# Optimization experiments

Measured on AMD Instinct MI355X. Metric: run time of the kernel, lower is better.

## Reference

```python
import jax, jax.numpy as jnp
import numpy as np
import math

B, N, DIN, H, D, M, K, E = 1, 30000, 128, 4, 64, 64, 6, 480000
TAU = 0.25
EPS = 1e-6  # numerical_stabilizer in softmax_kernel_transformation


def _make_projection(m, d, seed=0):
    # FAVOR+ projection: stacked QR-orthogonalized blocks, rows rescaled by
    # norms of iid gaussian rows (scaling == 0 branch of create_projection_matrix).
    rng = np.random.default_rng(seed)
    blocks, rows = [], 0
    while rows < m:
        q, _ = np.linalg.qr(rng.standard_normal((d, d)))
        blocks.append(q.T[: min(d, m - rows)])
        rows += d
    mat = np.vstack(blocks)
    mult = np.linalg.norm(rng.standard_normal((m, d)), axis=1)
    return jnp.asarray(mult[:, None] * mat, dtype=jnp.float32)


def setup_inputs() -> dict:
    key = jax.random.key(0)
    ks = jax.random.split(key, 10)
    f32 = jnp.float32
    return {
        "z": jax.random.normal(ks[0], (B, N, DIN), dtype=f32),
        "Wq_w": jax.random.normal(ks[1], (DIN, H * D), dtype=f32) * DIN ** -0.5,
        "Wq_b": jnp.zeros((H * D,), f32),
        "Wk_w": jax.random.normal(ks[2], (DIN, H * D), dtype=f32) * DIN ** -0.5,
        "Wk_b": jnp.zeros((H * D,), f32),
        "Wv_w": jax.random.normal(ks[3], (DIN, H * D), dtype=f32) * DIN ** -0.5,
        "Wv_b": jnp.zeros((H * D,), f32),
        "Wo_w": jax.random.normal(ks[4], (H * D, D), dtype=f32) * (H * D) ** -0.5,
        "Wo_b": jnp.zeros((D,), f32),
        "proj": _make_projection(M, D),
        "gumbels": jax.random.gumbel(ks[5], (N, B, H, K), dtype=f32),
        "edge_index": jax.random.randint(ks[6], (2, E), 0, N),
    }


def _softmax_kernel(data, proj, is_query):
    # softmax_kernel_transformation: positive random features for exp kernel.
    dn = 1.0 / jnp.sqrt(jnp.sqrt(jnp.asarray(data.shape[-1], data.dtype)))
    data = data * dn  # [B,N,H,D]
    ratio = 1.0 / jnp.sqrt(jnp.asarray(proj.shape[0], data.dtype))
    dd = jnp.einsum("bnhd,md->bnhm", data, proj)
    diag = jnp.sum(data * data, axis=-1, keepdims=True) * 0.5
    if is_query:
        mx = jnp.max(dd, axis=-1, keepdims=True)            # per-row max
    else:
        mx = jnp.max(dd, axis=(1, 3), keepdims=True)        # max over n and m
    return ratio * (jnp.exp(dd - diag - mx) + EPS)


def reference(z, Wq_w, Wq_b, Wk_w, Wk_b, Wv_w, Wv_b, Wo_w, Wo_b, proj, gumbels, edge_index):
    inv_sqrt_tau = 1.0 / math.sqrt(TAU)
    q = (z @ Wq_w + Wq_b).reshape(B, N, H, D) * inv_sqrt_tau
    k = (z @ Wk_w + Wk_b).reshape(B, N, H, D) * inv_sqrt_tau
    v = (z @ Wv_w + Wv_b).reshape(B, N, H, D)

    qp = jnp.transpose(_softmax_kernel(q, proj, True), (1, 0, 2, 3))   # [N,B,H,M]
    kp = jnp.transpose(_softmax_kernel(k, proj, False), (1, 0, 2, 3))  # [N,B,H,M]
    v = jnp.transpose(v, (1, 0, 2, 3))                                  # [N,B,H,D]

    g = gumbels / TAU                                                   # [N,B,H,K]
    kt = kp[:, :, :, None, :] * jnp.exp(g)[..., None]                   # [N,B,H,K,M]

    kvs = jnp.einsum("nbhkm,nbhd->bhkmd", kt, v)
    z_num = jnp.einsum("nbhm,bhkmd->nbhkd", qp, kvs)                    # [N,B,H,K,D]
    ks_sum = jnp.sum(kt, axis=0)                                        # [B,H,K,M]
    z_den = jnp.einsum("nbhm,bhkm->nbhk", qp, ks_sum)                   # [N,B,H,K]
    z_out = jnp.mean(z_num / z_den[..., None], axis=3)                  # [N,B,H,D]
    z_out = jnp.transpose(z_out, (1, 0, 2, 3))                          # [B,N,H,D]

    # edge attention weights (for edge loss), non-gumbel normalizer
    start, end = edge_index[0], edge_index[1]
    edge_num = jnp.einsum("ebhm,ebhm->ebh", qp[end], kp[start])         # [E,B,H]
    norm = jnp.einsum("nbhm,bhm->nbh", qp, jnp.sum(kp, axis=0))         # [N,B,H]
    A_weight = jnp.transpose(edge_num / norm[end], (1, 0, 2))           # [B,E,H]

    z_next = z_out.reshape(B, N, H * D) @ Wo_w + Wo_b                   # [B,N,D]
    return z_next, A_weight
```

## Files before the change

### kernel.cpp

```cpp
#include <hip/hip_runtime.h>
#include <hip/hip_bf16.h>

#define NN   30000
#define DIN  128
#define NHD  256
#define HH   4
#define DD   64
#define MM   64
#define KK   6
#define EE   480000
#define ZOFF 1920000
#define NCS   125
#define CHUNK 240
#define PITCH  30208
#define PITCH4 3776

typedef __attribute__((ext_vector_type(8))) short bf16x8;
typedef __attribute__((ext_vector_type(4))) float f32x4;
typedef __attribute__((ext_vector_type(2))) float f32x2;

__device__ __forceinline__ unsigned f2key(float f) {
    unsigned u = __float_as_uint(f);
    return (u & 0x80000000u) ? ~u : (u | 0x80000000u);
}
__device__ __forceinline__ float key2f(unsigned k) {
    return __uint_as_float((k & 0x80000000u) ? (k ^ 0x80000000u) : ~k);
}
__device__ __forceinline__ unsigned short f2bf(float f) {
    unsigned u = __float_as_uint(f);
    unsigned r = ((u >> 16) & 1u) + 0x7fffu;
    return (unsigned short)((u + r) >> 16);
}
__device__ __forceinline__ float bf2f(unsigned short u) {
    return __uint_as_float((unsigned)u << 16);
}
__device__ __forceinline__ unsigned char ftofp8(float x) {
    unsigned u = __float_as_uint(x);
    int e32 = (int)(u >> 23) - 127;
    if (e32 <= -7) {
        int m = (int)rintf(x * 512.f);
        return (unsigned char)m;
    }
    unsigned r = ((u >> 20) & 1u) + 0x7FFFFu;
    u += r;
    e32 = (int)(u >> 23) - 127;
    if (e32 > 8) return 0x7E;
    int m = (u >> 20) & 7;
    return (unsigned char)(((e32 + 7) << 3) | m);
}
__device__ __forceinline__ float fp8tof(unsigned char u) {
    int e = (u >> 3) & 15, m = u & 7;
    if (e == 0) return (float)m * 0.001953125f;
    return __uint_as_float((unsigned)((e + 120) << 23) | ((unsigned)m << 20));
}
__device__ __forceinline__ void fp8x4tof(unsigned w, float* o) {
#if __has_builtin(__builtin_amdgcn_cvt_pk_f32_fp8)
    f32x2 lo = __builtin_amdgcn_cvt_pk_f32_fp8((int)w, false);
    f32x2 hi = __builtin_amdgcn_cvt_pk_f32_fp8((int)w, true);
    o[0] = lo[0]; o[1] = lo[1]; o[2] = hi[0]; o[3] = hi[1];
#else
    o[0] = fp8tof((unsigned char)(w & 255));
    o[1] = fp8tof((unsigned char)((w >> 8) & 255));
    o[2] = fp8tof((unsigned char)((w >> 16) & 255));
    o[3] = fp8tof((unsigned char)((w >> 24) & 255));
#endif
}

__global__ void init_kernel(unsigned* gmax) {
    if (threadIdx.x < HH) gmax[threadIdx.x] = 0u;
}

__global__ __launch_bounds__(256) void zcast_kernel(
    const float* __restrict__ z, unsigned short* __restrict__ zh) {
    int idx = blockIdx.x * 256 + threadIdx.x;
    float4 v = ((const float4*)z)[idx];
    ushort4 u;
    u.x = f2bf(v.x); u.y = f2bf(v.y); u.z = f2bf(v.z); u.w = f2bf(v.w);
    ((ushort4*)zh)[idx] = u;
}

__global__ __launch_bounds__(256) void wtransp_kernel(
    const float* __restrict__ Wq, const float* __restrict__ Wk,
    const float* __restrict__ Wv, unsigned short* __restrict__ WT) {
    __shared__ unsigned short tl[64][72];
    const int t = threadIdx.x;
    const int kt = blockIdx.x & 1, ct = blockIdx.x >> 1;
    const int wi = blockIdx.y;
    const float* W = (wi == 0) ? Wq : (wi == 1) ? Wk : Wv;
    const float4* W4 = (const float4*)W;
    #pragma unroll
    for (int it = 0; it < 4; ++it) {
        int idx = t + it * 256;
        int r = idx >> 4, c4 = idx & 15;
        float4 v = W4[(kt * 64 + r) * 64 + ct * 16 + c4];
        tl[c4 * 4 + 0][r] = f2bf(v.x);
        tl[c4 * 4 + 1][r] = f2bf(v.y);
        tl[c4 * 4 + 2][r] = f2bf(v.z);
        tl[c4 * 4 + 3][r] = f2bf(v.w);
    }
    __syncthreads();
    uint4* d4 = (uint4*)WT;
    #pragma unroll
    for (int it = 0; it < 2; ++it) {
        int idx = t + it * 256;
        int m = idx >> 3, g = idx & 7;
        d4[((size_t)wi * 256 + ct * 64 + m) * 16 + kt * 8 + g] = *(uint4*)&tl[m][g * 8];
    }
}

__global__ void projcast_kernel(const float* __restrict__ proj,
                                unsigned short* __restrict__ projh) {
    int i = blockIdx.x * 256 + threadIdx.x;
    projh[i] = f2bf(proj[i] * 0.35355339059327373f);
}

__global__ __launch_bounds__(256) void qkv_mfma_kernel(
    const unsigned short* __restrict__ zh, const unsigned short* __restrict__ WT,
    const float* __restrict__ bq, const float* __restrict__ bk, const float* __restrict__ bv,
    unsigned short* __restrict__ qh, unsigned short* __restrict__ kh,
    unsigned short* __restrict__ vh) {
    __shared__ __align__(16) unsigned short zt[128 * 128];
    __shared__ __align__(16) unsigned short wt[64 * 128];
    const int t = threadIdx.x;
    const int n0 = blockIdx.x * 128;
    const int wi = blockIdx.y;
    const float sc = (wi == 2) ? 1.0f : 2.0f;
    const float* bias = (wi == 0) ? bq : (wi == 1) ? bk : bv;
    unsigned short* outp = (wi == 0) ? qh : (wi == 1) ? kh : vh;
    const uint4* zg = (const uint4*)zh;
    #pragma unroll
    for (int it = 0; it < 8; ++it) {
        int idx = t + it * 256;
        int row = idx >> 4, g = idx & 15;
        int n = n0 + row;
        uint4 v = make_uint4(0u, 0u, 0u, 0u);
        if (n < NN) v = zg[(size_t)n * 16 + g];
        *(uint4*)&zt[row * 128 + ((g ^ (row & 7)) * 8)] = v;
    }
    const uint4* wg = (const uint4*)WT + (size_t)wi * 4096;
    const int w = t >> 6, lane = t & 63, lrow = lane & 15, lk = lane >> 4;
    for (int cc = 0; cc < 4; ++cc) {
        __syncthreads();
        #pragma unroll
        for (int it = 0; it < 4; ++it) {
            int idx = t + it * 256;
            int r = idx >> 4, g = idx & 15;
            *(uint4*)&wt[r * 128 + ((g ^ (r & 7)) * 8)] = wg[(cc * 64 + r) * 16 + g];
        }
        __syncthreads();
        f32x4 acc[4][2];
        #pragma unroll
        for (int mt = 0; mt < 4; ++mt) {
            acc[mt][0] = (f32x4){0.f, 0.f, 0.f, 0.f};
            acc[mt][1] = (f32x4){0.f, 0.f, 0.f, 0.f};
        }
        #pragma unroll
        for (int ks = 0; ks < 4; ++ks) {
            const int g0 = ks * 4 + lk;
            bf16x8 a[4], b[2];
            #pragma unroll
            for (int mt = 0; mt < 4; ++mt) {
                int r = mt * 16 + lrow;
                a[mt] = *(const bf16x8*)&wt[r * 128 + ((g0 ^ (r & 7)) * 8)];
            }
            #pragma unroll
            for (int nt = 0; nt < 2; ++nt) {
                int node = (w * 2 + nt) * 16 + lrow;
                b[nt] = *(const bf16x8*)&zt[node * 128 + ((g0 ^ (node & 7)) * 8)];
            }
            #pragma unroll
            for (int mt = 0; mt < 4; ++mt)
                #pragma unroll
                for (int nt = 0; nt < 2; ++nt)
                    acc[mt][nt] = __builtin_amdgcn_mfma_f32_16x16x32_bf16(
                        a[mt], b[nt], acc[mt][nt], 0, 0, 0);
        }
        #pragma unroll
        for (int mt = 0; mt < 4; ++mt) {
            int cbase = cc * 64 + mt * 16 + lk * 4;
            float4 bi = *(const float4*)&bias[cbase];
            #pragma unroll
            for (int nt = 0; nt < 2; ++nt) {
                int n = n0 + (w * 2 + nt) * 16 + lrow;
                if (n < NN) {
                    ushort4 u;
                    u.x = f2bf((acc[mt][nt][0] + bi.x) * sc);
                    u.y = f2bf((acc[mt][nt][1] + bi.y) * sc);
                    u.z = f2bf((acc[mt][nt][2] + bi.z) * sc);
                    u.w = f2bf((acc[mt][nt][3] + bi.w) * sc);
                    *(ushort4*)&outp[(size_t)n * NHD + cbase] = u;
                }
            }
        }
    }
}

__global__ __launch_bounds__(256) void feat_mfma_kernel(
    unsigned short* __restrict__ qbh, const unsigned short* __restrict__ kh,
    float* __restrict__ kb, const unsigned short* __restrict__ projh,
    unsigned* __restrict__ gmax) {
    __shared__ __align__(16) unsigned short at[64 * 64];
    __shared__ __align__(16) unsigned short pb[64 * 64];
    __shared__ __align__(16) float ddt[64 * 68];
    __shared__ float diag_sh[64];
    __shared__ float wmax_sh[4];
    const int t = threadIdx.x;
    const int h = blockIdx.y;
    const int n0 = blockIdx.x * 64;
    const int tx = t & 15, ty = t >> 4;
    const uint4* pg = (const uint4*)projh;
    #pragma unroll
    for (int q = 0; q < 2; ++q) {
        int idx = t + q * 256;
        int m = idx >> 3, g = idx & 7;
        *(uint4*)&pb[m * 64 + ((g ^ (m & 7)) * 8)] = pg[idx];
    }
    const int w = t >> 6, lane = t & 63, lrow = lane & 15, lk = lane >> 4;
    const int arow = w * 16 + lrow;
    #pragma unroll
    for (int pass = 0; pass < 2; ++pass) {
        const uint4* src = (const uint4*)(pass ? kh : qbh);
        __syncthreads();
        #pragma unroll
        for (int q = 0; q < 2; ++q) {
            int idx = t + q * 256;
            int n = idx >> 3, g = idx & 7;
            uint4 v = make_uint4(0u, 0u, 0u, 0u);
            if (n0 + n < NN) v = src[(size_t)(n0 + n) * 32 + h * 8 + g];
            *(uint4*)&at[n * 64 + ((g ^ (n & 7)) * 8)] = v;
            const unsigned short* e8 = (const unsigned short*)&v;
            float ss = 0.f;
            #pragma unroll
            for (int j2 = 0; j2 < 8; ++j2) { float f = bf2f(e8[j2]); ss += f * f; }
            ss += __shfl_xor(ss, 1, 64);
            ss += __shfl_xor(ss, 2, 64);
            ss += __shfl_xor(ss, 4, 64);
            if (g == 0) diag_sh[n] = 0.0625f * ss;
        }
        __syncthreads();
        bf16x8 a0 = *(const bf16x8*)&at[arow * 64 + ((lk ^ (arow & 7)) * 8)];
        bf16x8 a1 = *(const bf16x8*)&at[arow * 64 + (((lk + 4) ^ (arow & 7)) * 8)];
        #pragma unroll
        for (int ct = 0; ct < 4; ++ct) {
            int brow = ct * 16 + lrow;
            bf16x8 b0 = *(const bf16x8*)&pb[brow * 64 + ((lk ^ (brow & 7)) * 8)];
            bf16x8 b1 = *(const bf16x8*)&pb[brow * 64 + (((lk + 4) ^ (brow & 7)) * 8)];
            f32x4 acc = {0.f, 0.f, 0.f, 0.f};
            acc = __builtin_amdgcn_mfma_f32_16x16x32_bf16(a0, b0, acc, 0, 0, 0);
            acc = __builtin_amdgcn_mfma_f32_16x16x32_bf16(a1, b1, acc, 0, 0, 0);
            #pragma unroll
            for (int r = 0; r < 4; ++r)
                ddt[(w * 16 + lk * 4 + r) * 68 + ct * 16 + lrow] = acc[r];
        }
        __syncthreads();
        if (pass == 0) {
            #pragma unroll
            for (int i = 0; i < 4; ++i) {
                int n = n0 + ty * 4 + i;
                float a_[4];
                #pragma unroll
                for (int j = 0; j < 4; ++j) a_[j] = ddt[(ty * 4 + i) * 68 + tx * 4 + j];
                float mx = fmaxf(fmaxf(a_[0], a_[1]), fmaxf(a_[2], a_[3]));
                mx = fmaxf(mx, __shfl_xor(mx, 1, 64));
                mx = fmaxf(mx, __shfl_xor(mx, 2, 64));
                mx = fmaxf(mx, __shfl_xor(mx, 4, 64));
                mx = fmaxf(mx, __shfl_xor(mx, 8, 64));
                if (n < NN) {
                    float dg = diag_sh[ty * 4 + i] + mx;
                    ushort4 u;
                    u.x = f2bf(0.125f * (__expf(a_[0] - dg) + 1e-6f));
                    u.y = f2bf(0.125f * (__expf(a_[1] - dg) + 1e-6f));
                    u.z = f2bf(0.125f * (__expf(a_[2] - dg) + 1e-6f));
                    u.w = f2bf(0.125f * (__expf(a_[3] - dg) + 1e-6f));
                    *(ushort4*)&qbh[(size_t)n * NHD + h * DD + tx * 4] = u;
                }
            }
        } else {
            float km = -3.4e38f;
            #pragma unroll
            for (int i = 0; i < 4; ++i) {
                int n = n0 + ty * 4 + i;
                if (n < NN) {
                    float a_[4];
                    #pragma unroll
                    for (int j = 0; j < 4; ++j) a_[j] = ddt[(ty * 4 + i) * 68 + tx * 4 + j];
                    float dg = diag_sh[ty * 4 + i];
                    float4 o;
                    o.x = a_[0] - dg; o.y = a_[1] - dg;
                    o.z = a_[2] - dg; o.w = a_[3] - dg;
                    *(float4*)&kb[(size_t)n * NHD + h * DD + tx * 4] = o;
                    km = fmaxf(km, fmaxf(fmaxf(a_[0], a_[1]), fmaxf(a_[2], a_[3])));
                }
            }
            #pragma unroll
            for (int off = 1; off < 64; off <<= 1) km = fmaxf(km, __shfl_xor(km, off, 64));
            if ((t & 63) == 0) wmax_sh[t >> 6] = km;
            __syncthreads();
            if (t == 0) {
                float m2 = fmaxf(fmaxf(wmax_sh[0], wmax_sh[1]), fmaxf(wmax_sh[2], wmax_sh[3]));
                atomicMax(&gmax[h], f2key(m2));
            }
        }
    }
}

__global__ __launch_bounds__(256) void kfin_tr_kernel(
    const float* __restrict__ kb, const unsigned* __restrict__ gmax,
    unsigned short* __restrict__ kbh, unsigned short* __restrict__ kbhT) {
    __shared__ unsigned short tl[64][72];
    const int t = threadIdx.x;
    const int n0 = blockIdx.x * 64;
    const int h = blockIdx.y;
    const float mx = key2f(gmax[h]);
    const float4* s4 = (const float4*)kb;
    #pragma unroll
    for (int it = 0; it < 4; ++it) {
        int idx = t + it * 256;
        int n = idx >> 4, c4 = idx & 15;
        ushort4 u = make_ushort4(0, 0, 0, 0);
        if (n0 + n < NN) {
            float4 v = s4[(size_t)(n0 + n) * 64 + h * 16 + c4];
            u.x = f2bf(0.125f * (__expf(v.x - mx) + 1e-6f));
            u.y = f2bf(0.125f * (__expf(v.y - mx) + 1e-6f));
            u.z = f2bf(0.125f * (__expf(v.z - mx) + 1e-6f));
            u.w = f2bf(0.125f * (__expf(v.w - mx) + 1e-6f));
            *(ushort4*)&kbh[(size_t)(n0 + n) * NHD + h * DD + c4 * 4] = u;
        }
        tl[c4 * 4 + 0][n] = u.x;
        tl[c4 * 4 + 1][n] = u.y;
        tl[c4 * 4 + 2][n] = u.z;
        tl[c4 * 4 + 3][n] = u.w;
    }
    __syncthreads();
    uint4* d4 = (uint4*)kbhT;
    #pragma unroll
    for (int it = 0; it < 2; ++it) {
        int idx = t + it * 256;
        int m = idx >> 3, g = idx & 7;
        d4[(size_t)(h * 64 + m) * PITCH4 + (n0 >> 3) + g] = *(uint4*)&tl[m][g * 8];
    }
}

__global__ __launch_bounds__(256) void transp_bf16_kernel(
    const unsigned short* __restrict__ src, unsigned short* __restrict__ dst) {
    __shared__ unsigned short tl[64][72];
    const int t = threadIdx.x;
    const int nt = blockIdx.x * 64;
    const int h = blockIdx.y;
    const uint4* s4 = (const uint4*)src;
    #pragma unroll
    for (int it = 0; it < 2; ++it) {
        int idx = t + it * 256;
        int n = idx >> 3, g = idx & 7;
        uint4 v = make_uint4(0u, 0u, 0u, 0u);
        if (nt + n < NN) v = s4[(size_t)(nt + n) * 32 + h * 8 + g];
        const unsigned short* e = (const unsigned short*)&v;
        #pragma unroll
        for (int j = 0; j < 8; ++j) tl[g * 8 + j][n] = e[j];
    }
    __syncthreads();
    uint4* d4 = (uint4*)dst;
    #pragma unroll
    for (int it = 0; it < 2; ++it) {
        int idx = t + it * 256;
        int m = idx >> 3, g = idx & 7;
        d4[(size_t)(h * 64 + m) * PITCH4 + (nt >> 3) + g] = *(uint4*)&tl[m][g * 8];
    }
}

__global__ __launch_bounds__(256) void fp8cast_kernel(
    const unsigned short* __restrict__ src, unsigned char* __restrict__ dst) {
    int idx = blockIdx.x * 256 + threadIdx.x;
    uint4 v = ((const uint4*)src)[idx];
    const unsigned short* e = (const unsigned short*)&v;
    unsigned char o[8];
    #pragma unroll
    for (int j = 0; j < 8; ++j) o[j] = ftofp8(bf2f(e[j]) * 2048.f);
    ((uint2*)dst)[idx] = *(uint2*)o;
}

__global__ __launch_bounds__(512) void kvs_kernel(
    const unsigned short* __restrict__ kbhT, const unsigned short* __restrict__ vbhT,
    const float* __restrict__ gum,
    unsigned short* __restrict__ kvsp, float* __restrict__ ksp, float* __restrict__ ksump) {
    __shared__ __align__(16) unsigned short va [64 * 64];
    __shared__ __align__(16) unsigned short kpw[KK][64 * 64];
    __shared__ float w_sh[KK][256];
    const int c = blockIdx.x, h = blockIdx.y;
    const int t = threadIdx.x;
    const int n0 = c * CHUNK;
    const int n1 = n0 + CHUNK;
    for (int i = t; i < 256; i += 512) {
        int n = n0 + i;
        bool ok = (i < CHUNK);
        #pragma unroll
        for (int k = 0; k < KK; ++k)
            w_sh[k][i] = ok ? __expf(gum[n * 24 + h * KK + k] * 4.0f) : 0.f;
    }
    const int m_ = t >> 3, g_ = t & 7;
    const int w = t >> 6, lane = t & 63, lrow = lane & 15, lk = lane >> 4;
    const int ds = w & 3, mh = w >> 2;
    const int arow = ds * 16 + lrow;
    f32x4 acc[KK][2];
    #pragma unroll
    for (int k = 0; k < KK; ++k) {
        acc[k][0] = (f32x4){0.f, 0.f, 0.f, 0.f};
        acc[k][1] = (f32x4){0.f, 0.f, 0.f, 0.f};
    }
    float ks_acc[KK] = {0.f, 0.f, 0.f, 0.f, 0.f, 0.f};
    float ksum_acc = 0.f;
    const uint4* kT4 = (const uint4*)kbhT;
    const uint4* vT4 = (const uint4*)vbhT;
    uint4 kvv = kT4[(size_t)(h * 64 + m_) * PITCH4 + (n0 >> 3) + g_];
    uint4 vvv = vT4[(size_t)(h * 64 + m_) * PITCH4 + (n0 >> 3) + g_];
    __syncthreads();
    #pragma unroll
    for (int s = 0; s < 4; ++s) {
        const int nb = n0 + s * 64;
        const int slot = g_ ^ (m_ & 7);
        *(uint4*)&va[m_ * 64 + slot * 8] = vvv;
        float kf[8];
        {
            const unsigned short* ke = (const unsigned short*)&kvv;
            float sl = 0.f;
            int nbase = nb + g_ * 8;
            #pragma unroll
            for (int e = 0; e < 8; ++e) {
                kf[e] = bf2f(ke[e]);
                if (nbase + e < n1) sl += kf[e];
            }
            sl += __shfl_xor(sl, 1, 64);
            sl += __shfl_xor(sl, 2, 64);
            sl += __shfl_xor(sl, 4, 64);
            if (g_ == 0) ksum_acc += sl;
        }
        if (s < 3) {
            const int nb2 = nb + 64;
            kvv = kT4[(size_t)(h * 64 + m_) * PITCH4 + (nb2 >> 3) + g_];
            vvv = vT4[(size_t)(h * 64 + m_) * PITCH4 + (nb2 >> 3) + g_];
        }
        const int bw = s * 64;
        const int gg = g_ ^ (m_ & 7);
        #pragma unroll
        for (int k = 0; k < KK; ++k) {
            unsigned short ov[8];
            float sl = 0.f;
            #pragma unroll
            for (int e = 0; e < 8; ++e) {
                float p = kf[e] * w_sh[k][bw + gg * 8 + e];
                sl += p;
                ov[e] = f2bf(p);
            }
            *(uint4*)&kpw[k][m_ * 64 + g_ * 8] = *(uint4*)ov;
            sl += __shfl_xor(sl, 1, 64);
            sl += __shfl_xor(sl, 2, 64);
            sl += __shfl_xor(sl, 4, 64);
            if (g_ == 0) ks_acc[k] += sl;
        }
        __syncthreads();
        bf16x8 a0 = *(const bf16x8*)&va[arow * 64 + ((lk ^ (arow & 7)) * 8)];
        bf16x8 a1 = *(const bf16x8*)&va[arow * 64 + (((lk + 4) ^ (arow & 7)) * 8)];
        #pragma unroll
        for (int k = 0; k < KK; ++k) {
            #pragma unroll
            for (int mt = 0; mt < 2; ++mt) {
                int m = (mh * 2 + mt) * 16 + lrow;
                bf16x8 b0 = *(const bf16x8*)&kpw[k][m * 64 + ((lk ^ (m & 7)) * 8)];
                bf16x8 b1 = *(const bf16x8*)&kpw[k][m * 64 + (((lk + 4) ^ (m & 7)) * 8)];
                acc[k][mt] = __builtin_amdgcn_mfma_f32_16x16x32_bf16(a0, b0, acc[k][mt], 0, 0, 0);
                acc[k][mt] = __builtin_amdgcn_mfma_f32_16x16x32_bf16(a1, b1, acc[k][mt], 0, 0, 0);
            }
        }
        __syncthreads();
    }
    const size_t cb = (size_t)(c * HH + h) * KK;
    #pragma unroll
    for (int k = 0; k < KK; ++k)
        #pragma unroll
        for (int mt = 0; mt < 2; ++mt) {
            int m = (mh * 2 + mt) * 16 + lrow;
            #pragma unroll
            for (int r = 0; r < 4; ++r) {
                int d = ds * 16 + lk * 4 + r;
                kvsp[(cb + k) * 4096 + d * 64 + m] = f2bf(acc[k][mt][r]);
            }
        }
    if (g_ == 0) {
        #pragma unroll
        for (int k = 0; k < KK; ++k)
            ksp[(cb + k) * 64 + m_] = ks_acc[k];
        ksump[(size_t)(c * HH + h) * 64 + m_] = ksum_acc;
    }
}

__global__ void reduce_kernel(const unsigned short* __restrict__ kvsp,
                              const float* __restrict__ ksp, const float* __restrict__ ksump,
                              unsigned short* __restrict__ kvshT, float* __restrict__ kss,
                              float* __restrict__ ksum) {
    int idx = blockIdx.x * 256 + threadIdx.x;
    if (idx < 98304) {
        float s = 0.f;
        for (int c = 0; c < NCS; ++c) s += bf2f(kvsp[c * 98304 + idx]);
        kvshT[idx] = f2bf(s);
    } else if (idx < 98304 + 1536) {
        int o = idx - 98304;
        float s = 0.f;
        for (int c = 0; c < NCS; ++c) s += ksp[c * 1536 + o];
        kss[o] = s;
    } else if (idx < 98304 + 1536 + 256) {
        int o = idx - 98304 - 1536;
        float s = 0.f;
        for (int c = 0; c < NCS; ++c) s += ksump[c * 256 + o];
        ksum[o] = s;
    }
}

__global__ __launch_bounds__(512) void znum_kernel(
    const unsigned short* __restrict__ qbh, const unsigned short* __restrict__ kvshT,
    const float* __restrict__ kss, const float* __restrict__ ksum,
    unsigned short* __restrict__ zouth, float* __restrict__ nrm) {
    __shared__ __align__(16) unsigned short qpa[64 * 64];
    __shared__ __align__(16) unsigned short bt[6 * 64 * 64];
    __shared__ __align__(16) unsigned short bbuf[16 * 72];
    __shared__ float zdi[64 * 6];
    const int t = threadIdx.x;
    const int h = blockIdx.y;
    const int n0 = blockIdx.x * 64;
    const uint4* qg = (const uint4*)qbh;
    {
        int row = t >> 3, c8 = t & 7;
        int n = n0 + row;
        uint4 v = make_uint4(0u, 0u, 0u, 0u);
        if (n < NN) v = qg[n * 32 + h * 8 + c8];
        *(uint4*)&qpa[row * 64 + ((c8 ^ (row & 7)) * 8)] = v;
    }
    const uint4* bg = (const uint4*)kvshT;
    #pragma unroll
    for (int q = 0; q < 6; ++q) {
        int idx = t + q * 512;
        int kd = idx >> 3, c8 = idx & 7;
        *(uint4*)&bt[kd * 64 + ((c8 ^ (kd & 7)) * 8)] = bg[h * 3072 + idx];
    }
    #pragma unroll
    for (int q = 0; q < 2; ++q) {
        int idx = t + q * 512;
        int col = idx >> 6, m = idx & 63;
        float v = 0.f;
        if (col < 6) v = kss[h * 384 + col * 64 + m];
        else if (col == 6) v = ksum[h * 64 + m];
        bbuf[col * 72 + m] = f2bf(v);
    }
    __syncthreads();
    const int w = t >> 6, lane = t & 63;
    const int lrow = lane & 15, lk = lane >> 4;
    const int w2 = w & 3, wh = w >> 2;
    const int arow = w2 * 16 + lrow;
    const int aswz = (arow & 7) << 3;
    bf16x8 a0 = *(const bf16x8*)&qpa[arow * 64 + ((lk * 8) ^ aswz)];
    bf16x8 a1 = *(const bf16x8*)&qpa[arow * 64 + ((lk * 8 + 32) ^ aswz)];
    if (wh == 0) {
        bf16x8 b0 = *(const bf16x8*)&bbuf[lrow * 72 + lk * 8];
        bf16x8 b1 = *(const bf16x8*)&bbuf[lrow * 72 + lk * 8 + 32];
        f32x4 acc = {0.f, 0.f, 0.f, 0.f};
        acc = __builtin_amdgcn_mfma_f32_16x16x32_bf16(a0, b0, acc, 0, 0, 0);
        acc = __builtin_amdgcn_mfma_f32_16x16x32_bf16(a1, b1, acc, 0, 0, 0);
        #pragma unroll
        for (int r = 0; r < 4; ++r) {
            int node = w2 * 16 + lk * 4 + r;
            if (lrow < 6) zdi[node * 6 + lrow] = 1.0f / acc[r];
            else if (lrow == 6) {
                int n = n0 + node;
                if (n < NN) nrm[n * HH + h] = acc[r];
            }
        }
    }
    __syncthreads();
    const float inv6 = 1.0f / 6.0f;
    #pragma unroll
    for (int dtt = 0; dtt < 2; ++dtt) {
        const int dt = wh * 2 + dtt;
        f32x4 outv = {0.f, 0.f, 0.f, 0.f};
        #pragma unroll
        for (int k = 0; k < KK; ++k) {
            int kd = k * 64 + dt * 16 + lrow;
            int sw = (kd & 7) << 3;
            bf16x8 b0 = *(const bf16x8*)&bt[kd * 64 + ((lk * 8) ^ sw)];
            bf16x8 b1 = *(const bf16x8*)&bt[kd * 64 + ((lk * 8 + 32) ^ sw)];
            f32x4 acc = {0.f, 0.f, 0.f, 0.f};
            acc = __builtin_amdgcn_mfma_f32_16x16x32_bf16(a0, b0, acc, 0, 0, 0);
            acc = __builtin_amdgcn_mfma_f32_16x16x32_bf16(a1, b1, acc, 0, 0, 0);
            #pragma unroll
            for (int r = 0; r < 4; ++r)
                outv[r] += zdi[(w2 * 16 + lk * 4 + r) * 6 + k] * acc[r];
        }
        #pragma unroll
        for (int r = 0; r < 4; ++r) {
            int n = n0 + w2 * 16 + lk * 4 + r;
            if (n < NN) zouth[(size_t)n * NHD + h * DD + dt * 16 + lrow] = f2bf(outv[r] * inv6);
        }
    }
}

__global__ __launch_bounds__(256) void outproj_kernel(
    const unsigned short* __restrict__ zouth, const float* __restrict__ Wo,
    const float* __restrict__ bo, float* __restrict__ out) {
    __shared__ float zsh[16][NHD];
    const int t = threadIdx.x;
    const int n0 = blockIdx.x * 16;
    const uint4* zg = (const uint4*)zouth;
    #pragma unroll
    for (int q = 0; q < 2; ++q) {
        int idx = t + q * 256;
        int row = idx >> 5, g = idx & 31;
        uint4 v = zg[(size_t)(n0 + row) * 32 + g];
        const unsigned short* e = (const unsigned short*)&v;
        #pragma unroll
        for (int j = 0; j < 8; ++j) zsh[row][g * 8 + j] = bf2f(e[j]);
    }
    __syncthreads();
    const int c = t & 63, g = t >> 6;
    float acc[4];
    #pragma unroll
    for (int i = 0; i < 4; ++i) acc[i] = bo[c];
    for (int r = 0; r < 256; ++r) {
        float w = Wo[r * 64 + c];
        #pragma unroll
        for (int i = 0; i < 4; ++i) acc[i] += zsh[g + 4 * i][r] * w;
    }
    #pragma unroll
    for (int i = 0; i < 4; ++i)
        out[(n0 + g + 4 * i) * 64 + c] = acc[i];
}

__global__ __launch_bounds__(256) void edge_fp8_kernel(
    const unsigned char* __restrict__ qb8, const unsigned char* __restrict__ kb8,
    const int* __restrict__ ei, const float* __restrict__ nrm,
    float* __restrict__ out) {
    const int t = threadIdx.x;
    const int li = t & 15;
    const int e = blockIdx.x * 16 + (t >> 4);
    const int s = ei[e], d = ei[EE + e];
    uint4 qv = ((const uint4*)qb8)[d * 16 + li];
    uint4 kv = ((const uint4*)kb8)[s * 16 + li];
    float qf[16], kf[16];
    fp8x4tof(qv.x, qf + 0);  fp8x4tof(qv.y, qf + 4);
    fp8x4tof(qv.z, qf + 8);  fp8x4tof(qv.w, qf + 12);
    fp8x4tof(kv.x, kf + 0);  fp8x4tof(kv.y, kf + 4);
    fp8x4tof(kv.z, kf + 8);  fp8x4tof(kv.w, kf + 12);
    float p = 0.f;
    #pragma unroll
    for (int i = 0; i < 16; ++i) p = fmaf(qf[i], kf[i], p);
    p += __shfl_xor(p, 1, 64);
    p += __shfl_xor(p, 2, 64);
    if ((li & 3) == 0) {
        int h = li >> 2;
        out[ZOFF + e * 4 + h] = p * (1.0f / (2048.f * 2048.f)) / nrm[d * HH + h];
    }
}

extern "C" void kernel_launch(void* const* d_in, const int* in_sizes, int n_in,
                              void* d_out, int out_size, void* d_ws, size_t ws_size,
                              hipStream_t stream) {
    (void)in_sizes; (void)n_in; (void)out_size;
    const float* z  = (const float*)d_in[0];
    const float* Wq = (const float*)d_in[1];
    const float* bq = (const float*)d_in[2];
    const float* Wk = (const float*)d_in[3];
    const float* bk = (const float*)d_in[4];
    const float* Wv = (const float*)d_in[5];
    const float* bv = (const float*)d_in[6];
    const float* Wo = (const float*)d_in[7];
    const float* bo = (const float*)d_in[8];
    const float* proj = (const float*)d_in[9];
    const float* gum  = (const float*)d_in[10];
    const int*   ei   = (const int*)d_in[11];
    float* out = (float*)d_out;
    float* ws = (float*)d_ws;

    if (ws_size / 4 < (size_t)38673348) return;

    float* kb    = ws + 7680000;
    unsigned char* qb8 = (unsigned char*)(ws + 7680000);
    unsigned char* kb8 = (unsigned char*)(ws + 9600000);
    unsigned short* zouth = (unsigned short*)(ws + 15360000);
    unsigned short* vh = (unsigned short*)(ws + 15360000);
    unsigned short* kvshT = (unsigned short*)(ws + 23040000);
    unsigned short* projh = (unsigned short*)(ws + 23089152);
    float* kss   = ws + 23138304;
    float* ksum  = ws + 23139840;
    float* nrm   = ws + 23140096;
    unsigned* gmax = (unsigned*)(ws + 23260096);
    unsigned short* qbh = (unsigned short*)(ws + 23260100);
    unsigned short* kbh = (unsigned short*)(ws + 27100100);
    unsigned short* kbhT = (unsigned short*)(ws + 30940100);
    unsigned short* vbhT = (unsigned short*)(ws + 34806724);
    unsigned short* zh = (unsigned short*)ws;
    unsigned short* WT = (unsigned short*)(ws + 3840000);
    float* ksp   = ws;
    float* ksump = ws + 192000;
    unsigned short* kvsp = (unsigned short*)(ws + 224000);

    init_kernel<<<1, 64, 0, stream>>>(gmax);
    zcast_kernel<<<3750, 256, 0, stream>>>(z, zh);
    wtransp_kernel<<<dim3(8, 3), 256, 0, stream>>>(Wq, Wk, Wv, WT);
    projcast_kernel<<<16, 256, 0, stream>>>(proj, projh);
    qkv_mfma_kernel<<<dim3(235, 3), 256, 0, stream>>>(zh, WT, bq, bk, bv, qbh, kbh, vh);
    transp_bf16_kernel<<<dim3(472, HH), 256, 0, stream>>>(vh, vbhT);
    feat_mfma_kernel<<<dim3(469, HH), 256, 0, stream>>>(qbh, kbh, kb, projh, gmax);
    kfin_tr_kernel<<<dim3(472, HH), 256, 0, stream>>>(kb, gmax, kbh, kbhT);
    fp8cast_kernel<<<3750, 256, 0, stream>>>(qbh, qb8);
    fp8cast_kernel<<<3750, 256, 0, stream>>>(kbh, kb8);
    kvs_kernel<<<dim3(NCS, HH), 512, 0, stream>>>(kbhT, vbhT, gum, kvsp, ksp, ksump);
    reduce_kernel<<<392, 256, 0, stream>>>(kvsp, ksp, ksump, kvshT, kss, ksum);
    znum_kernel<<<dim3(469, HH), 512, 0, stream>>>(qbh, kvshT, kss, ksum, zouth, nrm);
    outproj_kernel<<<1875, 256, 0, stream>>>(zouth, Wo, bo, out);
    edge_fp8_kernel<<<30000, 256, 0, stream>>>(qb8, kb8, ei, nrm, out);
}
```

Before: 214.9 us.

## Split kvs chunks into two half-blocks to double grid parallelism

```diff
diff --git a/kernel.cpp b/kernel.cpp
--- a/kernel.cpp
+++ b/kernel.cpp
@@ -11,6 +11,7 @@
 #define EE   480000
 #define ZOFF 1920000
 #define NCS   125
+#define NP    250
 #define CHUNK 240
 #define PITCH  30208
 #define PITCH4 3776
@@ -386,7 +387,8 @@
     __shared__ __align__(16) unsigned short va [64 * 64];
     __shared__ __align__(16) unsigned short kpw[KK][64 * 64];
     __shared__ float w_sh[KK][256];
-    const int c = blockIdx.x, h = blockIdx.y;
+    const int c2 = blockIdx.x, h = blockIdx.y;
+    const int c = c2 >> 1, z = c2 & 1;
     const int t = threadIdx.x;
     const int n0 = c * CHUNK;
     const int n1 = n0 + CHUNK;
@@ -411,12 +413,11 @@
     float ksum_acc = 0.f;
     const uint4* kT4 = (const uint4*)kbhT;
     const uint4* vT4 = (const uint4*)vbhT;
-    uint4 kvv = kT4[(size_t)(h * 64 + m_) * PITCH4 + (n0 >> 3) + g_];
-    uint4 vvv = vT4[(size_t)(h * 64 + m_) * PITCH4 + (n0 >> 3) + g_];
     __syncthreads();
-    #pragma unroll
-    for (int s = 0; s < 4; ++s) {
+    for (int s = z * 2; s < z * 2 + 2; ++s) {
         const int nb = n0 + s * 64;
+        uint4 kvv = kT4[(size_t)(h * 64 + m_) * PITCH4 + (nb >> 3) + g_];
+        uint4 vvv = vT4[(size_t)(h * 64 + m_) * PITCH4 + (nb >> 3) + g_];
         const int slot = g_ ^ (m_ & 7);
         *(uint4*)&va[m_ * 64 + slot * 8] = vvv;
         float kf[8];
@@ -434,11 +435,6 @@
             sl += __shfl_xor(sl, 4, 64);
             if (g_ == 0) ksum_acc += sl;
         }
-        if (s < 3) {
-            const int nb2 = nb + 64;
-            kvv = kT4[(size_t)(h * 64 + m_) * PITCH4 + (nb2 >> 3) + g_];
-            vvv = vT4[(size_t)(h * 64 + m_) * PITCH4 + (nb2 >> 3) + g_];
-        }
         const int bw = s * 64;
         const int gg = g_ ^ (m_ & 7);
         #pragma unroll
@@ -473,7 +469,7 @@
         }
         __syncthreads();
     }
-    const size_t cb = (size_t)(c * HH + h) * KK;
+    const size_t cb = (size_t)(c2 * HH + h) * KK;
     #pragma unroll
     for (int k = 0; k < KK; ++k)
         #pragma unroll
@@ -489,7 +485,7 @@
         #pragma unroll
         for (int k = 0; k < KK; ++k)
             ksp[(cb + k) * 64 + m_] = ks_acc[k];
-        ksump[(size_t)(c * HH + h) * 64 + m_] = ksum_acc;
+        ksump[(size_t)(c2 * HH + h) * 64 + m_] = ksum_acc;
     }
 }
 
@@ -500,17 +496,17 @@
     int idx = blockIdx.x * 256 + threadIdx.x;
     if (idx < 98304) {
         float s = 0.f;
-        for (int c = 0; c < NCS; ++c) s += bf2f(kvsp[c * 98304 + idx]);
+        for (int c = 0; c < NP; ++c) s += bf2f(kvsp[c * 98304 + idx]);
         kvshT[idx] = f2bf(s);
     } else if (idx < 98304 + 1536) {
         int o = idx - 98304;
         float s = 0.f;
-        for (int c = 0; c < NCS; ++c) s += ksp[c * 1536 + o];
+        for (int c = 0; c < NP; ++c) s += ksp[c * 1536 + o];
         kss[o] = s;
     } else if (idx < 98304 + 1536 + 256) {
         int o = idx - 98304 - 1536;
         float s = 0.f;
-        for (int c = 0; c < NCS; ++c) s += ksump[c * 256 + o];
+        for (int c = 0; c < NP; ++c) s += ksump[c * 256 + o];
         ksum[o] = s;
     }
 }
@@ -680,8 +676,6 @@
     if (ws_size / 4 < (size_t)38673348) return;
 
     float* kb    = ws + 7680000;
-    unsigned char* qb8 = (unsigned char*)(ws + 7680000);
-    unsigned char* kb8 = (unsigned char*)(ws + 9600000);
     unsigned short* zouth = (unsigned short*)(ws + 15360000);
     unsigned short* vh = (unsigned short*)(ws + 15360000);
     unsigned short* kvshT = (unsigned short*)(ws + 23040000);
@@ -696,9 +690,11 @@
     unsigned short* vbhT = (unsigned short*)(ws + 34806724);
     unsigned short* zh = (unsigned short*)ws;
     unsigned short* WT = (unsigned short*)(ws + 3840000);
-    float* ksp   = ws;
-    float* ksump = ws + 192000;
-    unsigned short* kvsp = (unsigned short*)(ws + 224000);
+    unsigned short* kvsp = (unsigned short*)(ws + 4000000);
+    float* ksp   = ws + 16300000;
+    float* ksump = ws + 16700000;
+    unsigned char* qb8 = (unsigned char*)ws;
+    unsigned char* kb8 = (unsigned char*)(ws + 1920000);
 
     init_kernel<<<1, 64, 0, stream>>>(gmax);
     zcast_kernel<<<3750, 256, 0, stream>>>(z, zh);
@@ -708,10 +704,10 @@
     transp_bf16_kernel<<<dim3(472, HH), 256, 0, stream>>>(vh, vbhT);
     feat_mfma_kernel<<<dim3(469, HH), 256, 0, stream>>>(qbh, kbh, kb, projh, gmax);
     kfin_tr_kernel<<<dim3(472, HH), 256, 0, stream>>>(kb, gmax, kbh, kbhT);
+    kvs_kernel<<<dim3(NP, HH), 512, 0, stream>>>(kbhT, vbhT, gum, kvsp, ksp, ksump);
+    reduce_kernel<<<392, 256, 0, stream>>>(kvsp, ksp, ksump, kvshT, kss, ksum);
     fp8cast_kernel<<<3750, 256, 0, stream>>>(qbh, qb8);
     fp8cast_kernel<<<3750, 256, 0, stream>>>(kbh, kb8);
-    kvs_kernel<<<dim3(NCS, HH), 512, 0, stream>>>(kbhT, vbhT, gum, kvsp, ksp, ksump);
-    reduce_kernel<<<392, 256, 0, stream>>>(kvsp, ksp, ksump, kvshT, kss, ksum);
     znum_kernel<<<dim3(469, HH), 512, 0, stream>>>(qbh, kvshT, kss, ksum, zouth, nrm);
     outproj_kernel<<<1875, 256, 0, stream>>>(zouth, Wo, bo, out);
     edge_fp8_kernel<<<30000, 256, 0, stream>>>(qb8, kb8, ei, nrm, out);
```

After: 224.2 us. +4.3%, slower.
